# Performance work log

Measured on AMD Instinct MI355X. Metric: run time of the kernel, lower is better.

The kernel has to match this reference:

```python
import jax, jax.numpy as jnp
import numpy as np

N_GT, N_NODES, N_SPECIES, N_EDGES, D, L = 512, 399, 200, 397, 64, 2


def setup_inputs() -> dict:
    rng = np.random.default_rng(0)
    # Random recursive trees: parent of node i is uniform in [0, i).
    par = (rng.random((N_GT, N_NODES - 1)) * np.arange(1, N_NODES)).astype(np.int64)
    child = np.broadcast_to(np.arange(1, N_NODES), (N_GT, N_NODES - 1))
    off = (np.arange(N_GT, dtype=np.int64) * N_NODES)[:, None]
    c = (child + off).ravel()
    p = (par + off).ravel()
    # Both directions, as in the original [2, 2E_gt] convention.
    edge_index = np.stack([np.concatenate([c, p]), np.concatenate([p, c])])
    sp = np.full(N_NODES, -1, dtype=np.int64)
    sp[:N_SPECIES] = np.arange(N_SPECIES)
    sp_ids = np.tile(sp, N_GT)
    leaf_mask = sp_ids >= 0
    batch_vec = np.repeat(np.arange(N_GT, dtype=np.int64), N_NODES)
    # Clades: random species subsets per species-tree edge, guaranteed nonempty.
    pe = rng.uniform(0.05, 0.5, (N_EDGES, 1))
    clade_mask = rng.random((N_EDGES, N_SPECIES)) < pe
    clade_mask[np.arange(N_EDGES), rng.integers(0, N_SPECIES, N_EDGES)] = True
    key = jax.random.key(0)
    ks = jax.random.split(key, 3)
    s = 1.0 / np.sqrt(D)
    return {
        "edge_index": jnp.asarray(edge_index),
        "sp_ids": jnp.asarray(sp_ids),
        "leaf_mask": jnp.asarray(leaf_mask),
        "batch_vec": jnp.asarray(batch_vec),
        "clade_mask": jnp.asarray(clade_mask),
        "n_gt": N_GT,
        "emb_table": jax.random.normal(ks[0], (N_SPECIES + 1, D), jnp.float32),
        "W1": jax.random.normal(ks[1], (L, D, D), jnp.float32) * s,
        "b1": jnp.zeros((L, D), jnp.float32),
        "W2": jax.random.normal(ks[2], (L, D, D), jnp.float32) * s,
        "b2": jnp.zeros((L, D), jnp.float32),
        "eps": jnp.zeros((L,), jnp.float32),  # GINConv train_eps init 0
        "ln_gamma": jnp.ones((L, D), jnp.float32),
        "ln_beta": jnp.zeros((L, D), jnp.float32),
    }


def _layernorm(x, g, b):
    mu = x.mean(-1, keepdims=True)
    var = ((x - mu) ** 2).mean(-1, keepdims=True)
    return (x - mu) * jax.lax.rsqrt(var + 1e-5) * g + b


def reference(edge_index, sp_ids, leaf_mask, batch_vec, clade_mask, n_gt,
              emb_table, W1, b1, W2, b2, eps, ln_gamma, ln_beta):
    n_nodes = sp_ids.shape[0]
    n_edges, n_species = clade_mask.shape
    d = emb_table.shape[1]
    # Species embedding (internal nodes -> extra row n_species).
    emb_ids = jnp.where(sp_ids < 0, n_species, sp_ids)
    x = emb_table[emb_ids]  # [Nn, D]
    src, dst = edge_index[0], edge_index[1]
    for l in range(W1.shape[0]):
        # GINConv: mlp((1+eps)*x + sum_neighbors x_j), residual, LayerNorm.
        msg = jax.ops.segment_sum(x[src], dst, num_segments=n_nodes)
        h = (1.0 + eps[l]) * x + msg
        h = jax.nn.relu(h @ W1[l] + b1[l]) @ W2[l] + b2[l]
        x = _layernorm(x + h, ln_gamma[l], ln_beta[l])
        # dropout is identity in eval mode
    # Species pooling: mean over valid leaves per (gene tree, species).
    w = (leaf_mask & (sp_ids >= 0)).astype(x.dtype)  # [Nn]
    comp = batch_vec * n_species + jnp.maximum(sp_ids, 0)
    pool_size = n_gt * n_species
    sums = jax.ops.segment_sum(x * w[:, None], comp, num_segments=pool_size)
    cnts = jax.ops.segment_sum(w, comp, num_segments=pool_size)
    pool = (sums / jnp.maximum(cnts, 1.0)[:, None]).reshape(n_gt, n_species, d)
    valid = (cnts > 0).astype(x.dtype).reshape(n_gt, n_species)  # [G, S]
    # Clade pooling per species-tree edge (vectorized over the per-edge loop).
    mf = clade_mask.astype(x.dtype)  # [E, S]
    csum = jnp.einsum('es,gsd->egd', mf, pool * valid[:, :, None])  # [E,G,D]
    ccnt = mf @ valid.T  # [E, G] valid-species count per (edge, gene tree)
    gt_means = csum / jnp.maximum(ccnt, 1.0)[:, :, None]
    has = (ccnt > 0).astype(x.dtype)  # gene trees with data for this edge
    n_v = has.sum(1)  # [E]
    mean = (gt_means * has[:, :, None]).sum(1) / jnp.maximum(n_v, 1.0)[:, None]
    diff = (gt_means - mean[:, None, :]) * has[:, :, None]
    var = (diff ** 2).sum(1) / jnp.maximum(n_v - 1.0, 1.0)[:, None]  # unbiased
    ok = (n_v > 1)[:, None]
    std = jnp.where(ok, jnp.sqrt(jnp.where(ok, var, 1.0)), 0.0)
    mean = jnp.where((n_v > 0)[:, None], mean, 0.0)
    return jnp.concatenate([mean, std], axis=-1)  # [n_edges, 2*D]
```

## Files before the change

### kernel.cpp

```cpp
#include <hip/hip_runtime.h>

#define NPG 399

typedef __bf16 bf16x8 __attribute__((ext_vector_type(8)));
typedef _Float16 half8 __attribute__((ext_vector_type(8)));
typedef float f32x4 __attribute__((ext_vector_type(4)));

__device__ __forceinline__ unsigned short f2bf(float f) {
  unsigned u = __float_as_uint(f);
  unsigned r = (u + 0x7FFFu + ((u >> 16) & 1u)) >> 16;
  return (unsigned short)r;
}
__device__ __forceinline__ int xel(int node, int dim) {
  return node * 64 + ((((dim >> 3)) ^ (node & 7)) << 3) + (dim & 7);
}

__global__ __launch_bounds__(256) void k_prep(const int* __restrict__ clade,
                                              const float* __restrict__ W1,
                                              const float* __restrict__ W2,
                                              unsigned short* __restrict__ mfA,
                                              unsigned* __restrict__ mfbits,
                                              _Float16* __restrict__ wswz,
                                              int n_edges, int n_species) {
  int stride = gridDim.x * 256;
  for (int idx = blockIdx.x * 256 + threadIdx.x; idx < 25 * 7 * 512;
       idx += stride) {
    int fi = idx >> 9, within = idx & 511;
    int mt = fi / 7, kt = fi % 7;
    int l = within >> 3, j = within & 7;
    int e = mt * 16 + (l & 15);
    int s = kt * 32 + ((l >> 4) & 3) * 8 + j;
    unsigned short v = 0;
    if (e < n_edges && s < n_species && clade[(size_t)e * n_species + s] != 0)
      v = 0x3F80;
    mfA[idx] = v;
  }
  for (int idx = blockIdx.x * 256 + threadIdx.x; idx < 400 * 8; idx += stride) {
    int e = idx >> 3, w = idx & 7;
    unsigned bits = 0;
    if (e < n_edges && w < 7) {
      for (int b = 0; b < 32; ++b) {
        int s = w * 32 + b;
        if (s < n_species && clade[(size_t)e * n_species + s] != 0)
          bits |= 1u << b;
      }
    }
    mfbits[idx] = bits;
  }
  for (int idx = blockIdx.x * 256 + threadIdx.x; idx < 16384; idx += stride) {
    int li = idx >> 12;
    int k = (idx >> 6) & 63, n = idx & 63;
    int frag = (k >> 5) * 4 + (n >> 4);
    int ln = ((k >> 3) & 3) * 16 + (n & 15);
    int j = k & 7;
    int l = li >> 1;
    const float* Ws = (li & 1) ? W2 : W1;
    wswz[li * 4096 + frag * 512 + ln * 8 + j] = (_Float16)Ws[l * 4096 + k * 64 + n];
  }
}

__global__ __launch_bounds__(512, 4) void k_tree(
    const float* __restrict__ emb, const int* __restrict__ sp,
    const int* __restrict__ leaf, const int* __restrict__ src,
    const int* __restrict__ dst, const _Float16* __restrict__ wswz,
    const float* __restrict__ b1, const float* __restrict__ b2,
    const float* __restrict__ eps_p, const float* __restrict__ gam,
    const float* __restrict__ bet, unsigned short* __restrict__ pool_swz,
    unsigned* __restrict__ valid_bits, int npg, int n_species) {
  __shared__ __attribute__((aligned(16))) _Float16 sA[NPG * 64];
  __shared__ __attribute__((aligned(16))) _Float16 sB[NPG * 64];
  __shared__ __attribute__((aligned(16))) _Float16 sT[8][1024];
  __shared__ int sStart[NPG + 1];
  __shared__ int sChild[NPG - 1];
  __shared__ int sPar[NPG];
  __shared__ int sCnt[NPG];

  int g = blockIdx.x, tid = threadIdx.x;
  int base = g * npg, nEt = npg - 1, ebase = g * nEt;
  int w = tid >> 6, lane = tid & 63;
  int cc = lane & 15, gq = lane >> 4;

  for (int i = tid; i < npg + 1; i += 512) sStart[i] = 0;
  for (int i = tid; i < npg; i += 512) sCnt[i] = 0;
  __syncthreads();
  for (int idx = tid; idx < npg * 8; idx += 512) {
    int node = idx >> 3, ch = idx & 7;
    int s = sp[base + node];
    int row = (s < 0) ? n_species : s;
    float4 v0 = reinterpret_cast<const float4*>(emb)[row * 16 + ch * 2];
    float4 v1 = reinterpret_cast<const float4*>(emb)[row * 16 + ch * 2 + 1];
    half8 h;
    h[0] = (_Float16)v0.x; h[1] = (_Float16)v0.y;
    h[2] = (_Float16)v0.z; h[3] = (_Float16)v0.w;
    h[4] = (_Float16)v1.x; h[5] = (_Float16)v1.y;
    h[6] = (_Float16)v1.z; h[7] = (_Float16)v1.w;
    *reinterpret_cast<half8*>(&sA[node * 64 + ((ch ^ (node & 7)) << 3)]) = h;
  }
  for (int i = tid; i < nEt; i += 512) {
    int c = src[ebase + i] - base;
    int p = dst[ebase + i] - base;
    sPar[c] = p;
    atomicAdd(&sStart[p + 1], 1);
  }
  __syncthreads();
  if (w == 0) {
    int run = 0;
    for (int chunk = 0; chunk * 64 < npg + 1; ++chunk) {
      int idx = chunk * 64 + lane;
      int v = (idx < npg + 1) ? sStart[idx] : 0;
      for (int off = 1; off < 64; off <<= 1) {
        int t2 = __shfl_up(v, off);
        if (lane >= off) v += t2;
      }
      v += run;
      if (idx < npg + 1) sStart[idx] = v;
      run = __shfl(v, 63);
    }
  }
  __syncthreads();
  for (int c = tid + 1; c < npg; c += 512) {
    int p = sPar[c];
    int pos = sStart[p] + atomicAdd(&sCnt[p], 1);
    sChild[pos] = c;
  }
  __syncthreads();

  _Float16* tb = sT[w];
  int t0w = w * 3;
  int t1w = (w == 7) ? 25 : t0w + 3;
  for (int l = 0; l < 2; ++l) {
    const _Float16* xin = l ? sB : sA;
    _Float16* xout = l ? sA : sB;
    const half8* xin8 = reinterpret_cast<const half8*>(xin);
    float e1 = 1.0f + eps_p[l];
    float b1v[4], b2v[4], gv[4], bv[4];
#pragma unroll
    for (int nt = 0; nt < 4; ++nt) {
      b1v[nt] = b1[l * 64 + cc + 16 * nt];
      b2v[nt] = b2[l * 64 + cc + 16 * nt];
      gv[nt] = gam[l * 64 + cc + 16 * nt];
      bv[nt] = bet[l * 64 + cc + 16 * nt];
    }
    const half8* B1 = reinterpret_cast<const half8*>(wswz + (l * 2 + 0) * 4096);
    const half8* B2 = reinterpret_cast<const half8*>(wswz + (l * 2 + 1) * 4096);
    for (int t = t0w; t < t1w; ++t) {
      int n0 = t * 16;
      int node = n0 + cc;
      bool vn = node < npg;
      int nd2 = vn ? node : 0;
      int j0v = vn ? sStart[nd2] : 0;
      int cnt = vn ? (sStart[nd2 + 1] - j0v) : 0;
      half8 s0 = xin8[nd2 * 8 + (gq ^ (nd2 & 7))];
      half8 s1 = xin8[nd2 * 8 + ((4 + gq) ^ (nd2 & 7))];
      bool hasp = vn && node > 0;
      int pr = hasp ? sPar[nd2] : 0;
      half8 p0 = xin8[pr * 8 + (gq ^ (pr & 7))];
      half8 p1 = xin8[pr * 8 + ((4 + gq) ^ (pr & 7))];
      float a0f[8], a1f[8];
#pragma unroll
      for (int d = 0; d < 8; ++d) {
        a0f[d] = e1 * (float)s0[d] + (hasp ? (float)p0[d] : 0.f);
        a1f[d] = e1 * (float)s1[d] + (hasp ? (float)p1[d] : 0.f);
      }
      int cmax = cnt;
#pragma unroll
      for (int off = 1; off < 64; off <<= 1)
        cmax = max(cmax, __shfl_xor(cmax, off));
      cmax = __builtin_amdgcn_readfirstlane(cmax);
#pragma unroll 2
      for (int k = 0; k < cmax; ++k) {
        bool act = k < cnt;
        int jidx = act ? (j0v + k) : 0;
        int c = sChild[jidx];
        half8 v0 = xin8[c * 8 + (gq ^ (c & 7))];
        half8 v1 = xin8[c * 8 + ((4 + gq) ^ (c & 7))];
        if (act) {
#pragma unroll
          for (int d = 0; d < 8; ++d) {
            a0f[d] += (float)v0[d];
            a1f[d] += (float)v1[d];
          }
        }
      }
      half8 a0, a1;
#pragma unroll
      for (int d = 0; d < 8; ++d) {
        a0[d] = (_Float16)a0f[d];
        a1[d] = (_Float16)a1f[d];
      }
      f32x4 tacc[4];
#pragma unroll
      for (int nt = 0; nt < 4; ++nt) tacc[nt] = (f32x4){0.f, 0.f, 0.f, 0.f};
#pragma unroll
      for (int nt = 0; nt < 4; ++nt) {
        tacc[nt] = __builtin_amdgcn_mfma_f32_16x16x32_f16(
            a0, B1[nt * 64 + lane], tacc[nt], 0, 0, 0);
        tacc[nt] = __builtin_amdgcn_mfma_f32_16x16x32_f16(
            a1, B1[(4 + nt) * 64 + lane], tacc[nt], 0, 0, 0);
      }
#pragma unroll
      for (int nt = 0; nt < 4; ++nt)
#pragma unroll
        for (int r = 0; r < 4; ++r) {
          int m = gq * 4 + r;
          tb[m * 64 + ((cc + 16 * nt) ^ ((m & 7) << 3))] =
              (_Float16)fmaxf(tacc[nt][r] + b1v[nt], 0.f);
        }
      int sw = (cc & 7) << 3;
      half8 c0 =
          *reinterpret_cast<const half8*>(&tb[cc * 64 + ((gq * 8) ^ sw)]);
      half8 c1 =
          *reinterpret_cast<const half8*>(&tb[cc * 64 + ((32 + gq * 8) ^ sw)]);
      f32x4 hacc[4];
#pragma unroll
      for (int nt = 0; nt < 4; ++nt) hacc[nt] = (f32x4){0.f, 0.f, 0.f, 0.f};
#pragma unroll
      for (int nt = 0; nt < 4; ++nt) {
        hacc[nt] = __builtin_amdgcn_mfma_f32_16x16x32_f16(
            c0, B2[nt * 64 + lane], hacc[nt], 0, 0, 0);
        hacc[nt] = __builtin_amdgcn_mfma_f32_16x16x32_f16(
            c1, B2[(4 + nt) * 64 + lane], hacc[nt], 0, 0, 0);
      }
      float y[4][4];
#pragma unroll
      for (int r = 0; r < 4; ++r) {
        int nd3 = n0 + gq * 4 + r;
        bool v3 = nd3 < npg;
        int nds = v3 ? nd3 : 0;
#pragma unroll
        for (int nt = 0; nt < 4; ++nt) {
          float xv = (float)xin[xel(nds, cc + 16 * nt)];
          y[r][nt] = (v3 ? xv : 0.f) + hacc[nt][r] + b2v[nt];
        }
      }
#pragma unroll
      for (int r = 0; r < 4; ++r) {
        float s = y[r][0] + y[r][1] + y[r][2] + y[r][3];
        s += __shfl_xor(s, 1);
        s += __shfl_xor(s, 2);
        s += __shfl_xor(s, 4);
        s += __shfl_xor(s, 8);
        float mu = s * (1.f / 64.f);
        float d0 = y[r][0] - mu, d1 = y[r][1] - mu;
        float d2 = y[r][2] - mu, d3 = y[r][3] - mu;
        float v = d0 * d0 + d1 * d1 + d2 * d2 + d3 * d3;
        v += __shfl_xor(v, 1);
        v += __shfl_xor(v, 2);
        v += __shfl_xor(v, 4);
        v += __shfl_xor(v, 8);
        float iv = rsqrtf(v * (1.f / 64.f) + 1e-5f);
        int nd3 = n0 + gq * 4 + r;
        if (nd3 < npg) {
#pragma unroll
          for (int nt = 0; nt < 4; ++nt)
            xout[xel(nd3, cc + 16 * nt)] =
                (_Float16)((y[r][nt] - mu) * iv * gv[nt] + bv[nt]);
        }
      }
    }
    __syncthreads();
  }

  for (int i = tid; i < n_species + 1; i += 512) sStart[i] = 0;
  for (int i = tid; i < n_species; i += 512) sCnt[i] = 0;
  __syncthreads();
  for (int i = tid; i < npg; i += 512) {
    int s = sp[base + i];
    if (s >= 0 && leaf[base + i] != 0) atomicAdd(&sStart[s + 1], 1);
  }
  __syncthreads();
  if (w == 0) {
    int run = 0;
    for (int chunk = 0; chunk * 64 < n_species + 1; ++chunk) {
      int idx = chunk * 64 + lane;
      int v = (idx < n_species + 1) ? sStart[idx] : 0;
      for (int off = 1; off < 64; off <<= 1) {
        int t2 = __shfl_up(v, off);
        if (lane >= off) v += t2;
      }
      v += run;
      if (idx < n_species + 1) sStart[idx] = v;
      run = __shfl(v, 63);
    }
  }
  __syncthreads();
  for (int i = tid; i < npg; i += 512) {
    int s = sp[base + i];
    if (s >= 0 && leaf[base + i] != 0) {
      int pos = sStart[s] + atomicAdd(&sCnt[s], 1);
      sPar[pos] = i;
    }
  }
  __syncthreads();
  unsigned short* pg = pool_swz + (size_t)g * 14336;
  for (int idx = tid; idx < 224 * 8; idx += 512) {
    int s = idx >> 3, dc = idx & 7;
    float sum[8] = {0.f, 0.f, 0.f, 0.f, 0.f, 0.f, 0.f, 0.f};
    int cntv = 0;
    if (s < n_species) {
      int j0 = sStart[s], j1 = sStart[s + 1];
      cntv = j1 - j0;
      for (int j2 = j0; j2 < j1; ++j2) {
        int nd = sPar[j2];
        half8 v = *reinterpret_cast<const half8*>(
            &sA[nd * 64 + ((dc ^ (nd & 7)) << 3)]);
#pragma unroll
        for (int dd = 0; dd < 8; ++dd) sum[dd] += (float)v[dd];
      }
    }
    float invc = (cntv > 0) ? 1.f / (float)cntv : 0.f;
#pragma unroll
    for (int dd = 0; dd < 8; ++dd) {
      int d = dc * 8 + dd;
      int frag = (s >> 5) * 4 + (d >> 4);
      int ln = ((s >> 3) & 3) * 16 + (d & 15);
      pg[frag * 512 + ln * 8 + (s & 7)] = f2bf(sum[dd] * invc);
    }
  }
  if (tid < 7) {
    unsigned bits = 0;
    for (int b = 0; b < 32; ++b) {
      int s = tid * 32 + b;
      if (s < n_species && sStart[s + 1] > sStart[s]) bits |= 1u << b;
    }
    valid_bits[(size_t)g * 8 + tid] = bits;
  }
}

__global__ __launch_bounds__(512) void k_gm2(
    const unsigned short* __restrict__ pool_swz,
    const unsigned* __restrict__ valid_bits,
    const unsigned short* __restrict__ mfA, const unsigned* __restrict__ mfbits,
    _Float16* __restrict__ gmat, float* __restrict__ has, int n_edges,
    int n_gt) {
  __shared__ __attribute__((aligned(16))) unsigned short sBf[14336];
  __shared__ float sInv[400];
  __shared__ float sHas[400];
  int g = blockIdx.x;
  int tid = threadIdx.x;
  const float4* src4 =
      reinterpret_cast<const float4*>(pool_swz + (size_t)g * 14336);
  float4* dst4 = reinterpret_cast<float4*>(sBf);
  for (int i = tid; i < 1792; i += 512) dst4[i] = src4[i];
  unsigned vb[7];
#pragma unroll
  for (int w2 = 0; w2 < 7; ++w2) vb[w2] = valid_bits[(size_t)g * 8 + w2];
  for (int e = tid; e < 400; e += 512) {
    unsigned cc = 0;
#pragma unroll
    for (int w2 = 0; w2 < 7; ++w2) cc += __popc(mfbits[e * 8 + w2] & vb[w2]);
    sInv[e] = 1.f / (float)max(cc, 1u);
    sHas[e] = (cc > 0) ? 1.f : 0.f;
  }
  __syncthreads();
  int w = tid >> 6, lane = tid & 63;
  const bf16x8* A = reinterpret_cast<const bf16x8*>(mfA);
  const bf16x8* Bb = reinterpret_cast<const bf16x8*>(sBf);
  for (int mt = w; mt < 25; mt += 8) {
    bf16x8 af[7];
#pragma unroll
    for (int kt = 0; kt < 7; ++kt) af[kt] = A[(mt * 7 + kt) * 64 + lane];
    f32x4 acc0 = {0.f, 0.f, 0.f, 0.f};
    f32x4 acc1 = {0.f, 0.f, 0.f, 0.f};
    f32x4 acc2 = {0.f, 0.f, 0.f, 0.f};
    f32x4 acc3 = {0.f, 0.f, 0.f, 0.f};
#pragma unroll
    for (int kt = 0; kt < 7; ++kt) {
      const bf16x8* B = Bb + kt * 256 + lane;
      acc0 = __builtin_amdgcn_mfma_f32_16x16x32_bf16(af[kt], B[0], acc0, 0, 0, 0);
      acc1 = __builtin_amdgcn_mfma_f32_16x16x32_bf16(af[kt], B[64], acc1, 0, 0, 0);
      acc2 = __builtin_amdgcn_mfma_f32_16x16x32_bf16(af[kt], B[128], acc2, 0, 0, 0);
      acc3 = __builtin_amdgcn_mfma_f32_16x16x32_bf16(af[kt], B[192], acc3, 0, 0, 0);
    }
    int rbase = mt * 16 + (lane >> 4) * 4;
    int col = lane & 15;
#pragma unroll
    for (int r = 0; r < 4; ++r) {
      int e = rbase + r;
      if (e >= n_edges) continue;
      float inv = sInv[e];
      _Float16* gp = gmat + ((size_t)e * n_gt + g) * 64 + col;
      gp[0] = (_Float16)(acc0[r] * inv);
      gp[16] = (_Float16)(acc1[r] * inv);
      gp[32] = (_Float16)(acc2[r] * inv);
      gp[48] = (_Float16)(acc3[r] * inv);
      if (col == 0) has[(size_t)e * n_gt + g] = sHas[e];
    }
  }
}

__global__ __launch_bounds__(256) void k_stat2(const _Float16* __restrict__ gmat,
                                               const float* __restrict__ has,
                                               float* __restrict__ part,
                                               int n_gt) {
  __shared__ float red1[4][64];
  __shared__ float red2[4][64];
  __shared__ float redn[4];
  int b = blockIdx.x;
  int e = b >> 2, q = b & 3;
  int tid = threadIdx.x, w = tid >> 6, lane = tid & 63;
  const _Float16* ge = gmat + ((size_t)e * n_gt + q * 128) * 64;
  const float* he = has + (size_t)e * n_gt + q * 128;
  float S1 = 0.f, S2 = 0.f, nv = 0.f;
  for (int i = w; i < 128; i += 4) {
    float h = he[i];
    float v = (float)ge[i * 64 + lane];
    S1 += h * v;
    S2 += h * v * v;
    nv += h;
  }
  red1[w][lane] = S1;
  red2[w][lane] = S2;
  if (lane == 0) redn[w] = nv;
  __syncthreads();
  if (w == 0) {
    float s1 = 0.f, s2 = 0.f, n_v = 0.f;
#pragma unroll
    for (int j = 0; j < 4; ++j) {
      s1 += red1[j][lane];
      s2 += red2[j][lane];
      n_v += redn[j];
    }
    float* p = part + (size_t)b * 130;
    p[lane] = s1;
    p[64 + lane] = s2;
    if (lane == 0) p[128] = n_v;
  }
}

__global__ __launch_bounds__(64) void k_fin(const float* __restrict__ part,
                                            float* __restrict__ out) {
  int e = blockIdx.x;
  int lane = threadIdx.x;
  float s1 = 0.f, s2 = 0.f, n_v = 0.f;
#pragma unroll
  for (int q = 0; q < 4; ++q) {
    const float* p = part + (size_t)(e * 4 + q) * 130;
    s1 += p[lane];
    s2 += p[64 + lane];
    n_v += p[128];
  }
  float mean = s1 / fmaxf(n_v, 1.f);
  float var = (s2 - s1 * s1 / fmaxf(n_v, 1.f)) / fmaxf(n_v - 1.f, 1.f);
  float stdv = (n_v > 1.f) ? sqrtf(fmaxf(var, 0.f)) : 0.f;
  out[(size_t)e * 128 + lane] = (n_v > 0.f) ? mean : 0.f;
  out[(size_t)e * 128 + 64 + lane] = stdv;
}

extern "C" void kernel_launch(void* const* d_in, const int* in_sizes, int n_in,
                              void* d_out, int out_size, void* d_ws, size_t ws_size,
                              hipStream_t stream) {
  (void)n_in; (void)out_size; (void)ws_size;
  const int* edge_index = (const int*)d_in[0];
  const int* sp_ids = (const int*)d_in[1];
  const int* leaf_mask = (const int*)d_in[2];
  const int* clade_mask = (const int*)d_in[4];
  const float* emb = (const float*)d_in[6];
  const float* W1 = (const float*)d_in[7];
  const float* b1 = (const float*)d_in[8];
  const float* W2 = (const float*)d_in[9];
  const float* b2 = (const float*)d_in[10];
  const float* eps = (const float*)d_in[11];
  const float* lng = (const float*)d_in[12];
  const float* lnb = (const float*)d_in[13];
  float* out = (float*)d_out;

  const int n_nodes = in_sizes[1];
  const int nE = in_sizes[0] / 2;
  const int n_species = in_sizes[6] / 64 - 1;
  const int n_edges = in_sizes[4] / n_species;
  const int n_gt = 512;
  const int npg = n_nodes / n_gt;

  const int* src = edge_index;
  const int* dst = edge_index + nE;

  _Float16* gmat = (_Float16*)d_ws;
  size_t gsz =
      ((size_t)n_edges * n_gt * 64 * sizeof(_Float16) + 255ul) & ~255ul;
  float* has = (float*)((char*)d_ws + gsz);
  size_t hsz = ((size_t)n_edges * n_gt * sizeof(float) + 255ul) & ~255ul;
  unsigned short* mfA = (unsigned short*)((char*)d_ws + gsz + hsz);
  size_t masz = ((size_t)25 * 7 * 512 * sizeof(unsigned short) + 255ul) & ~255ul;
  unsigned* mfbits = (unsigned*)((char*)d_ws + gsz + hsz + masz);
  size_t mbsz = ((size_t)400 * 8 * sizeof(unsigned) + 255ul) & ~255ul;
  float* part = (float*)((char*)d_ws + gsz + hsz + masz + mbsz);
  size_t psz = ((size_t)n_edges * 4 * 130 * sizeof(float) + 255ul) & ~255ul;
  unsigned short* pool_swz =
      (unsigned short*)((char*)d_ws + gsz + hsz + masz + mbsz + psz);
  size_t poolsz = ((size_t)n_gt * 14336 * sizeof(unsigned short) + 255ul) & ~255ul;
  unsigned* valid_bits =
      (unsigned*)((char*)d_ws + gsz + hsz + masz + mbsz + psz + poolsz);
  size_t vbsz = ((size_t)n_gt * 8 * sizeof(unsigned) + 255ul) & ~255ul;
  _Float16* wswz = (_Float16*)((char*)d_ws + gsz + hsz + masz + mbsz + psz +
                               poolsz + vbsz);

  k_prep<<<64, 256, 0, stream>>>(clade_mask, W1, W2, mfA, mfbits, wswz,
                                 n_edges, n_species);
  k_tree<<<n_gt, 512, 0, stream>>>(emb, sp_ids, leaf_mask, src, dst, wswz, b1,
                                   b2, eps, lng, lnb, pool_swz, valid_bits,
                                   npg, n_species);
  k_gm2<<<n_gt, 512, 0, stream>>>(pool_swz, valid_bits, mfA, mfbits, gmat,
                                  has, n_edges, n_gt);
  k_stat2<<<n_edges * 4, 256, 0, stream>>>(gmat, has, part, n_gt);
  k_fin<<<n_edges, 64, 0, stream>>>(part, out);
}
```

Measured before the change: 123.8 us.

## Drop second LDS ping-pong buffer by staging layer outputs through global scratch

Removes the sB shared-memory buffer from the tree GNN kernel. Each layer's normalized output is staged through the per-warp tile buffer and written coalesced to a global scratch array. After a barrier it is copied back into sA for the next layer. This cuts LDS use per block (about 51KB each of sA and sB) so more blocks can be resident per CU. The cost is extra global write/read traffic and one more barrier per layer.

```diff
diff --git a/kernel.cpp b/kernel.cpp
--- a/kernel.cpp
+++ b/kernel.cpp
@@ -55,7 +55,8 @@
     int j = k & 7;
     int l = li >> 1;
     const float* Ws = (li & 1) ? W2 : W1;
-    wswz[li * 4096 + frag * 512 + ln * 8 + j] = (_Float16)Ws[l * 4096 + k * 64 + n];
+    wswz[li * 4096 + frag * 512 + ln * 8 + j] =
+        (_Float16)Ws[l * 4096 + k * 64 + n];
   }
 }
 
@@ -65,10 +66,10 @@
     const int* __restrict__ dst, const _Float16* __restrict__ wswz,
     const float* __restrict__ b1, const float* __restrict__ b2,
     const float* __restrict__ eps_p, const float* __restrict__ gam,
-    const float* __restrict__ bet, unsigned short* __restrict__ pool_swz,
-    unsigned* __restrict__ valid_bits, int npg, int n_species) {
+    const float* __restrict__ bet, _Float16* __restrict__ gx,
+    unsigned short* __restrict__ pool_swz, unsigned* __restrict__ valid_bits,
+    int npg, int n_species) {
   __shared__ __attribute__((aligned(16))) _Float16 sA[NPG * 64];
-  __shared__ __attribute__((aligned(16))) _Float16 sB[NPG * 64];
   __shared__ __attribute__((aligned(16))) _Float16 sT[8][1024];
   __shared__ int sStart[NPG + 1];
   __shared__ int sChild[NPG - 1];
@@ -128,10 +129,10 @@
   _Float16* tb = sT[w];
   int t0w = w * 3;
   int t1w = (w == 7) ? 25 : t0w + 3;
+  const half8* xin8 = reinterpret_cast<const half8*>(sA);
+  _Float16* gxg = gx + (size_t)base * 64;
+  half8* gxg8 = reinterpret_cast<half8*>(gxg);
   for (int l = 0; l < 2; ++l) {
-    const _Float16* xin = l ? sB : sA;
-    _Float16* xout = l ? sA : sB;
-    const half8* xin8 = reinterpret_cast<const half8*>(xin);
     float e1 = 1.0f + eps_p[l];
     float b1v[4], b2v[4], gv[4], bv[4];
 #pragma unroll
@@ -229,7 +230,7 @@
         int nds = v3 ? nd3 : 0;
 #pragma unroll
         for (int nt = 0; nt < 4; ++nt) {
-          float xv = (float)xin[xel(nds, cc + 16 * nt)];
+          float xv = (float)sA[xel(nds, cc + 16 * nt)];
           y[r][nt] = (v3 ? xv : 0.f) + hacc[nt][r] + b2v[nt];
         }
       }
@@ -249,14 +250,27 @@
         v += __shfl_xor(v, 4);
         v += __shfl_xor(v, 8);
         float iv = rsqrtf(v * (1.f / 64.f) + 1e-5f);
-        int nd3 = n0 + gq * 4 + r;
-        if (nd3 < npg) {
-#pragma unroll
-          for (int nt = 0; nt < 4; ++nt)
-            xout[xel(nd3, cc + 16 * nt)] =
-                (_Float16)((y[r][nt] - mu) * iv * gv[nt] + bv[nt]);
-        }
-      }
+        int m = gq * 4 + r;
+#pragma unroll
+        for (int nt = 0; nt < 4; ++nt)
+          tb[m * 64 + ((cc + 16 * nt) ^ ((m & 7) << 3))] =
+              (_Float16)((y[r][nt] - mu) * iv * gv[nt] + bv[nt]);
+      }
+#pragma unroll
+      for (int it = 0; it < 2; ++it) {
+        int idx = it * 64 + lane;
+        int m = idx >> 3, ch = idx & 7;
+        int nd = n0 + m;
+        if (nd < npg)
+          gxg8[nd * 8 + ch] = *reinterpret_cast<const half8*>(
+              &tb[m * 64 + ((ch ^ (m & 7)) << 3)]);
+      }
+    }
+    __syncthreads();
+    for (int idx = tid; idx < npg * 8; idx += 512) {
+      int node = idx >> 3, ch = idx & 7;
+      *reinterpret_cast<half8*>(&sA[node * 64 + ((ch ^ (node & 7)) << 3)]) =
+          gxg8[node * 8 + ch];
     }
     __syncthreads();
   }
@@ -475,30 +489,29 @@
   const int* src = edge_index;
   const int* dst = edge_index + nE;
 
-  _Float16* gmat = (_Float16*)d_ws;
-  size_t gsz =
-      ((size_t)n_edges * n_gt * 64 * sizeof(_Float16) + 255ul) & ~255ul;
-  float* has = (float*)((char*)d_ws + gsz);
-  size_t hsz = ((size_t)n_edges * n_gt * sizeof(float) + 255ul) & ~255ul;
-  unsigned short* mfA = (unsigned short*)((char*)d_ws + gsz + hsz);
-  size_t masz = ((size_t)25 * 7 * 512 * sizeof(unsigned short) + 255ul) & ~255ul;
-  unsigned* mfbits = (unsigned*)((char*)d_ws + gsz + hsz + masz);
-  size_t mbsz = ((size_t)400 * 8 * sizeof(unsigned) + 255ul) & ~255ul;
-  float* part = (float*)((char*)d_ws + gsz + hsz + masz + mbsz);
-  size_t psz = ((size_t)n_edges * 4 * 130 * sizeof(float) + 255ul) & ~255ul;
-  unsigned short* pool_swz =
-      (unsigned short*)((char*)d_ws + gsz + hsz + masz + mbsz + psz);
-  size_t poolsz = ((size_t)n_gt * 14336 * sizeof(unsigned short) + 255ul) & ~255ul;
-  unsigned* valid_bits =
-      (unsigned*)((char*)d_ws + gsz + hsz + masz + mbsz + psz + poolsz);
-  size_t vbsz = ((size_t)n_gt * 8 * sizeof(unsigned) + 255ul) & ~255ul;
-  _Float16* wswz = (_Float16*)((char*)d_ws + gsz + hsz + masz + mbsz + psz +
-                               poolsz + vbsz);
+  char* p = (char*)d_ws;
+  _Float16* gmat = (_Float16*)p;
+  p += ((size_t)n_edges * n_gt * 64 * sizeof(_Float16) + 255ul) & ~255ul;
+  float* has = (float*)p;
+  p += ((size_t)n_edges * n_gt * sizeof(float) + 255ul) & ~255ul;
+  unsigned short* mfA = (unsigned short*)p;
+  p += ((size_t)25 * 7 * 512 * sizeof(unsigned short) + 255ul) & ~255ul;
+  unsigned* mfbits = (unsigned*)p;
+  p += ((size_t)400 * 8 * sizeof(unsigned) + 255ul) & ~255ul;
+  float* part = (float*)p;
+  p += ((size_t)n_edges * 4 * 130 * sizeof(float) + 255ul) & ~255ul;
+  unsigned short* pool_swz = (unsigned short*)p;
+  p += ((size_t)n_gt * 14336 * sizeof(unsigned short) + 255ul) & ~255ul;
+  unsigned* valid_bits = (unsigned*)p;
+  p += ((size_t)n_gt * 8 * sizeof(unsigned) + 255ul) & ~255ul;
+  _Float16* wswz = (_Float16*)p;
+  p += ((size_t)16384 * sizeof(_Float16) + 255ul) & ~255ul;
+  _Float16* gx = (_Float16*)p;
 
   k_prep<<<64, 256, 0, stream>>>(clade_mask, W1, W2, mfA, mfbits, wswz,
                                  n_edges, n_species);
   k_tree<<<n_gt, 512, 0, stream>>>(emb, sp_ids, leaf_mask, src, dst, wswz, b1,
-                                   b2, eps, lng, lnb, pool_swz, valid_bits,
+                                   b2, eps, lng, lnb, gx, pool_swz, valid_bits,
                                    npg, n_species);
   k_gm2<<<n_gt, 512, 0, stream>>>(pool_swz, valid_bits, mfA, mfbits, gmat,
                                   has, n_edges, n_gt);
```

Measured after the change: 143.4 us. 1.16x slower.
